# Kernel optimization log

Hardware: AMD Instinct MI355X
Metric: run time of the kernel (lower is better)

Reference implementation:

```python
import jax, jax.numpy as jnp
import numpy as np

N = 50000   # nodes
E = 800000  # edges
D = 128     # input_dim == hidden_dim
R = 8       # num_relations
B = 2       # num_blocks


def setup_inputs() -> dict:
    key = jax.random.key(0)
    ks = jax.random.split(key, 9)
    x = jax.random.normal(ks[0], (N, D), dtype=jnp.float32)
    edge_index = jax.random.randint(ks[1], (2, E), 0, N, dtype=jnp.int32)
    edge_type = jax.random.randint(ks[2], (E,), 0, R, dtype=jnp.int32)
    s_blk = 1.0 / np.sqrt(D // B)
    s_root = 1.0 / np.sqrt(D)
    W1 = jax.random.normal(ks[3], (R, B, D // B, D // B), dtype=jnp.float32) * s_blk
    root1 = jax.random.normal(ks[4], (D, D), dtype=jnp.float32) * s_root
    b1 = jnp.zeros((D,), dtype=jnp.float32)
    W2 = jax.random.normal(ks[5], (R, B, D // B, D // B), dtype=jnp.float32) * s_blk
    root2 = jax.random.normal(ks[6], (D, D), dtype=jnp.float32) * s_root
    b2 = jnp.zeros((D,), dtype=jnp.float32)
    return {"x": x, "edge_index": edge_index, "edge_type": edge_type,
            "W1": W1, "root1": root1, "b1": b1,
            "W2": W2, "root2": root2, "b2": b2}


def rgcn_conv(x, src, dst, etype, W, root, bias):
    # PyG RGCNConv (num_blocks mode): per-relation MEAN aggregation of source
    # features, block-diagonal transform, summed over relations, plus root + bias.
    # Transform is linear, so aggregate first (saves per-edge matmuls).
    n = x.shape[0]
    r, b, ib, ob = W.shape
    xs = x[src]                                   # [E, d_in] gather
    seg = dst * r + etype                          # fused (node, relation) id
    sums = jax.ops.segment_sum(xs, seg, num_segments=n * r)        # [n*r, d_in]
    cnt = jax.ops.segment_sum(jnp.ones((xs.shape[0],), xs.dtype), seg,
                              num_segments=n * r)                   # [n*r]
    mean = sums / jnp.maximum(cnt, 1.0)[:, None]   # zero where no edges
    agg = mean.reshape(n, r, b, ib)                # [n, R, blocks, in/blocks]
    out = jnp.einsum('nrbc,rbcd->nbd', agg, W).reshape(n, b * ob)
    return out + x @ root + bias


def reference(x, edge_index, edge_type, W1, root1, b1, W2, root2, b2):
    src, dst = edge_index[0], edge_index[1]
    h = jax.nn.relu(rgcn_conv(x, src, dst, edge_type, W1, root1, b1))
    # dropout(p=0.2) is identity in eval mode (reference uses eval semantics)
    return rgcn_conv(h, src, dst, edge_type, W2, root2, b2)
```

## Files before the change

### kernel.cpp

```cpp
#include <hip/hip_runtime.h>

#define NN 50000
#define EE 800000
#define DD 128
#define RR 8
#define CELLS (NN * RR)
#define TILE_N 64
#define NBLK ((NN + TILE_N - 1) / TILE_N)
#define SCAN_CHUNK 1024
#define SCAN_BLOCKS ((CELLS + SCAN_CHUNK - 1) / SCAN_CHUNK)

typedef __attribute__((ext_vector_type(4))) float f32x4;
typedef __attribute__((ext_vector_type(8))) short s16x8;
union ABu { uint4 q; s16x8 v; };


__device__ __forceinline__ unsigned int packbf2(float a, float b) {
    unsigned int ua = __float_as_uint(a);
    unsigned int ub = __float_as_uint(b);
    ua = (ua + 0x7fffu + ((ua >> 16) & 1u)) >> 16;
    ub = (ub + 0x7fffu + ((ub >> 16) & 1u)) & 0xffff0000u;
    return ua | ub;
}

__device__ __forceinline__ void upadd16(float* sA, uint4 a, uint4 b) {
    unsigned int u[8] = {a.x, a.y, a.z, a.w, b.x, b.y, b.z, b.w};
#pragma unroll
    for (int j = 0; j < 8; ++j) {
        sA[2 * j]     += __uint_as_float(u[j] << 16);
        sA[2 * j + 1] += __uint_as_float(u[j] & 0xffff0000u);
    }
}

#define NB_A ((NN * 32 + 255) / 256)
#define NB_B 128
#define NB_C 32
#define NB_D ((EE + 255) / 256)

__global__ void prep_fused(const float* __restrict__ x, unsigned int* __restrict__ xb,
                           const float* __restrict__ W1, const float* __restrict__ W2,
                           unsigned int* __restrict__ Wb1, unsigned int* __restrict__ Wb2,
                           const float* __restrict__ r1, const float* __restrict__ r2,
                           unsigned int* __restrict__ rb1, unsigned int* __restrict__ rb2,
                           const int* __restrict__ dst, const int* __restrict__ et,
                           int* __restrict__ cnt) {
    int bid = blockIdx.x, tid = threadIdx.x;
    if (bid < NB_A) {
        int i = bid * 256 + tid;
        if (i < NN * 32) {
            float4 v = ((const float4*)x)[i];
            ((uint2*)xb)[i] = make_uint2(packbf2(v.x, v.y), packbf2(v.z, v.w));
        }
    } else if (bid < NB_A + NB_B) {
        int i = (bid - NB_A) * 256 + tid;
        int n = i & 63, kp = (i >> 6) & 31, rb = i >> 11;
        int s0 = (rb * 64 + 2 * kp) * 64 + n;
        int s1 = (rb * 64 + 2 * kp + 1) * 64 + n;
        Wb1[((rb * 64 + n) * 32) + kp] = packbf2(W1[s0], W1[s1]);
        Wb2[((rb * 64 + n) * 32) + kp] = packbf2(W2[s0], W2[s1]);
    } else if (bid < NB_A + NB_B + NB_C) {
        int i = (bid - NB_A - NB_B) * 256 + tid;
        int n = i & 127, kp = i >> 7;
        int s0 = (2 * kp) * 128 + n, s1 = (2 * kp + 1) * 128 + n;
        rb1[n * 64 + kp] = packbf2(r1[s0], r1[s1]);
        rb2[n * 64 + kp] = packbf2(r2[s0], r2[s1]);
    } else {
        int e = (bid - NB_A - NB_B - NB_C) * 256 + tid;
        if (e < EE) atomicAdd(&cnt[et[e] * NN + dst[e]], 1);
    }
}


__global__ __launch_bounds__(256) void scan1(const int* __restrict__ cnt,
                                             int* __restrict__ off, int* __restrict__ bsum) {
    __shared__ int s[256];
    int tid = threadIdx.x;
    int base = blockIdx.x * SCAN_CHUNK + tid * 4;
    int v[4];
#pragma unroll
    for (int i = 0; i < 4; ++i) v[i] = (base + i < CELLS) ? cnt[base + i] : 0;
    int tot = v[0] + v[1] + v[2] + v[3];
    s[tid] = tot;
    __syncthreads();
    for (int d = 1; d < 256; d <<= 1) {
        int t = (tid >= d) ? s[tid - d] : 0;
        __syncthreads();
        s[tid] += t;
        __syncthreads();
    }
    int excl = s[tid] - tot;
    if (tid == 255) bsum[blockIdx.x] = s[255];
    int run = excl;
#pragma unroll
    for (int i = 0; i < 4; ++i) {
        if (base + i < CELLS) off[base + i] = run;
        run += v[i];
    }
}

__global__ __launch_bounds__(256) void scan3(int* __restrict__ off, const int* __restrict__ bsum,
                                             int* __restrict__ cur) {
    __shared__ int red[256];
    int tid = threadIdx.x, bid = blockIdx.x;
    int a = 0;
    for (int i = tid; i < bid; i += 256) a += bsum[i];
    red[tid] = a;
    __syncthreads();
#pragma unroll
    for (int d = 128; d > 0; d >>= 1) {
        if (tid < d) red[tid] += red[tid + d];
        __syncthreads();
    }
    int add = red[0];
    int base = bid * SCAN_CHUNK + tid * 4;
#pragma unroll
    for (int i = 0; i < 4; ++i) {
        int c = base + i;
        if (c < CELLS) {
            int o = off[c] + add;
            off[c] = o;
            cur[c] = o;
        }
    }
    if (bid == 0 && tid == 0) off[CELLS] = EE;
}

__global__ void cell_scatter(const int* __restrict__ src, const int* __restrict__ dst,
                             const int* __restrict__ et, int* __restrict__ cur,
                             int* __restrict__ esrc) {
    int e = blockIdx.x * blockDim.x + threadIdx.x;
    if (e < EE) {
        int cell = et[e] * NN + dst[e];
        int pos = atomicAdd(&cur[cell], 1);
        esrc[pos] = src[e];
    }
}

__global__ __launch_bounds__(512, 8) void gather_cells(
    const unsigned int* __restrict__ xgb, const int* __restrict__ esrc,
    const int* __restrict__ off, unsigned int* __restrict__ AT) {

    int bid = blockIdx.x;
    int r = bid / NBLK, tb = bid - r * NBLK;
    int n0 = tb * TILE_N;
    int tid = threadIdx.x;
    int e = tid & 63, q = tid >> 6;
    int node = n0 + e;

    float sA[16];
#pragma unroll
    for (int i = 0; i < 16; ++i) sA[i] = 0.f;

    int ne = 0;
    if (node < NN) {
        int cell = r * NN + node;
        int o = off[cell];
        ne = off[cell + 1] - o;
        int t2 = 0;
        for (; t2 + 2 <= ne; t2 += 2) {
            int s0 = esrc[o + t2], s1 = esrc[o + t2 + 1];
            const uint4* p0 = (const uint4*)(xgb + (size_t)s0 * 64 + q * 8);
            const uint4* p1 = (const uint4*)(xgb + (size_t)s1 * 64 + q * 8);
            uint4 A0 = p0[0], A1 = p0[1];
            uint4 B0 = p1[0], B1 = p1[1];
            upadd16(sA, A0, A1);
            upadd16(sA, B0, B1);
        }
        if (t2 < ne) {
            int s0 = esrc[o + t2];
            const uint4* p0 = (const uint4*)(xgb + (size_t)s0 * 64 + q * 8);
            uint4 A0 = p0[0], A1 = p0[1];
            upadd16(sA, A0, A1);
        }
    }
    float sc = 1.0f / (float)max(ne, 1);

    unsigned int* dst = AT + ((size_t)bid << 12);
#pragma unroll
    for (int i = 0; i < 8; ++i)
        dst[(8 * q + i) * 64 + e] = packbf2(sA[2 * i] * sc, sA[2 * i + 1] * sc);
}

template <int RELU, int WRITEF, int WRITEB>
__global__ __launch_bounds__(512, 4) void gemm_fused(
    const unsigned int* __restrict__ xgb, const unsigned int* __restrict__ AT,
    const unsigned int* __restrict__ Wb, const unsigned int* __restrict__ rootb,
    const float* __restrict__ bias, float* __restrict__ outf,
    unsigned int* __restrict__ outb) {

    __shared__ unsigned int SH[8320];
    unsigned int* MT = SH;

    int tid = threadIdx.x;
    int tb = blockIdx.x;
    int n0 = tb * TILE_N;
    int e = tid & 63, q = tid >> 6;
    int w = q, l = e;
    int quad = l >> 4, li = l & 15;
    int b = w >> 2;
    int nloc = (w & 3) * 16 + li;

    f32x4 acc[4];
    {
        float bb = bias[16 * w + li];
#pragma unroll
        for (int mt = 0; mt < 4; ++mt) {
            acc[mt][0] = bb; acc[mt][1] = bb; acc[mt][2] = bb; acc[mt][3] = bb;
        }
    }

    int node = n0 + e;

#define MFMA_BLOCK(rr) do {                                                           \
    const uint4* WbB = (const uint4*)(Wb + (((size_t)(rr) * 2 + b) * 64) * 32);       \
    _Pragma("unroll") for (int kc = 0; kc < 2; ++kc) {                                \
        ABu bf; bf.q = WbB[nloc * 8 + 4 * kc + quad];                                 \
        _Pragma("unroll") for (int mt = 0; mt < 4; ++mt) {                            \
            ABu af; int base_ = (32 * b + 16 * kc + 4 * quad) * 67 + 16 * mt + li;    \
            af.q.x = MT[base_];       af.q.y = MT[base_ + 67];                        \
            af.q.z = MT[base_ + 134]; af.q.w = MT[base_ + 201];                       \
            acc[mt] = __builtin_amdgcn_mfma_f32_16x16x32_bf16(af.v, bf.v, acc[mt], 0, 0, 0); \
        } } } while (0)

#pragma unroll
    for (int r = 0; r < RR; ++r) {
        const unsigned int* at = AT + (((size_t)(r * NBLK + tb)) << 12) + (8 * q) * 64 + e;
        unsigned int tv[8];
#pragma unroll
        for (int i = 0; i < 8; ++i) tv[i] = at[i * 64];

        __syncthreads();
#pragma unroll
        for (int i = 0; i < 8; ++i) MT[(8 * q + i) * 67 + e] = tv[i];
        __syncthreads();
        MFMA_BLOCK(r);
    }
    __syncthreads();

    if (node < NN) {
        const uint4* xr = (const uint4*)(xgb + (size_t)node * 64 + q * 8);
        uint4 X0 = xr[0], X1 = xr[1];
        MT[(8 * q + 0) * 67 + e] = X0.x;
        MT[(8 * q + 1) * 67 + e] = X0.y;
        MT[(8 * q + 2) * 67 + e] = X0.z;
        MT[(8 * q + 3) * 67 + e] = X0.w;
        MT[(8 * q + 4) * 67 + e] = X1.x;
        MT[(8 * q + 5) * 67 + e] = X1.y;
        MT[(8 * q + 6) * 67 + e] = X1.z;
        MT[(8 * q + 7) * 67 + e] = X1.w;
    } else {
#pragma unroll
        for (int i = 0; i < 8; ++i) MT[(8 * q + i) * 67 + e] = 0u;
    }
    __syncthreads();

    const uint4* RbB = (const uint4*)rootb;
#pragma unroll
    for (int kc = 0; kc < 4; ++kc) {
        ABu bf;
        bf.q = RbB[(16 * w + li) * 16 + 4 * kc + quad];
#pragma unroll
        for (int mt = 0; mt < 4; ++mt) {
            ABu af;
            int base = (16 * kc + 4 * quad) * 67 + 16 * mt + li;
            af.q.x = MT[base]; af.q.y = MT[base + 67];
            af.q.z = MT[base + 134]; af.q.w = MT[base + 201];
            acc[mt] = __builtin_amdgcn_mfma_f32_16x16x32_bf16(af.v, bf.v, acc[mt], 0, 0, 0);
        }
    }
    __syncthreads();

    float* OF = (float*)SH;
#pragma unroll
    for (int mt = 0; mt < 4; ++mt)
#pragma unroll
        for (int reg = 0; reg < 4; ++reg)
            OF[(16 * mt + 4 * quad + reg) * 130 + 16 * w + li] = acc[mt][reg];
    __syncthreads();

    if (WRITEB) {
        int p = tid & 63, rg = tid >> 6;
#pragma unroll 4
        for (int it = 0; it < 8; ++it) {
            int ee = it * 8 + rg, row = n0 + ee;
            if (row < NN) {
                float v0 = OF[ee * 130 + 2 * p], v1 = OF[ee * 130 + 2 * p + 1];
                if (RELU) { v0 = fmaxf(v0, 0.f); v1 = fmaxf(v1, 0.f); }
                outb[(size_t)row * 64 + p] = packbf2(v0, v1);
            }
        }
    }
    if (WRITEF) {
        int d4 = (tid & 31) * 4, rg = tid >> 5;
#pragma unroll 4
        for (int it = 0; it < 4; ++it) {
            int ee = it * 16 + rg, row = n0 + ee;
            if (row < NN) {
                float4 v = make_float4(OF[ee * 130 + d4], OF[ee * 130 + d4 + 1],
                                       OF[ee * 130 + d4 + 2], OF[ee * 130 + d4 + 3]);
                if (RELU) {
                    v.x = fmaxf(v.x, 0.f); v.y = fmaxf(v.y, 0.f);
                    v.z = fmaxf(v.z, 0.f); v.w = fmaxf(v.w, 0.f);
                }
                *(float4*)(outf + (size_t)row * DD + d4) = v;
            }
        }
    }
#undef MFMA_BLOCK
}


extern "C" void kernel_launch(void* const* d_in, const int* in_sizes, int n_in,
                              void* d_out, int out_size, void* d_ws, size_t ws_size,
                              hipStream_t stream) {
    const float* x     = (const float*)d_in[0];
    const int*   ei    = (const int*)d_in[1];
    const int*   src   = ei;
    const int*   dstp  = ei + EE;
    const int*   et    = (const int*)d_in[2];
    const float* W1    = (const float*)d_in[3];
    const float* root1 = (const float*)d_in[4];
    const float* b1    = (const float*)d_in[5];
    const float* W2    = (const float*)d_in[6];
    const float* root2 = (const float*)d_in[7];
    const float* b2    = (const float*)d_in[8];
    float* out = (float*)d_out;

    unsigned int* xb  = (unsigned int*)d_ws;
    unsigned int* hb  = xb + (size_t)NN * 64;
    int* cnt  = (int*)(hb + (size_t)NN * 64);
    int* off  = cnt + CELLS;
    int* cur  = off + CELLS + 1;
    int* bsum = cur + CELLS;
    int* esrc = bsum + 512;
    unsigned int* Wb1 = (unsigned int*)(esrc + EE);
    unsigned int* Wb2 = Wb1 + 32768;
    unsigned int* rb1 = Wb2 + 32768;
    unsigned int* rb2 = rb1 + 8192;
    unsigned int* AT  = rb2 + 8192;

    hipMemsetAsync(cnt, 0, CELLS * sizeof(int), stream);
    prep_fused<<<NB_A + NB_B + NB_C + NB_D, 256, 0, stream>>>(
        x, xb, W1, W2, Wb1, Wb2, root1, root2, rb1, rb2, dstp, et, cnt);
    scan1<<<SCAN_BLOCKS, 256, 0, stream>>>(cnt, off, bsum);
    scan3<<<SCAN_BLOCKS, 256, 0, stream>>>(off, bsum, cur);
    cell_scatter<<<(EE + 255) / 256, 256, 0, stream>>>(src, dstp, et, cur, esrc);

    gather_cells<<<RR * NBLK, 512, 0, stream>>>(xb, esrc, off, AT);
    gemm_fused<1, 0, 1><<<NBLK, 512, 0, stream>>>(xb, AT, Wb1, rb1, b1, nullptr, hb);
    gather_cells<<<RR * NBLK, 512, 0, stream>>>(hb, esrc, off, AT);
    gemm_fused<0, 1, 0><<<NBLK, 512, 0, stream>>>(hb, AT, Wb2, rb2, b2, out, nullptr);
}
```

Baseline: 345.2 us.

## Remap gather threads so each node row is read by eight contiguous lanes

Changes the gather kernel's thread mapping so 8 consecutive lanes load one source node's full 256-byte bf16 row, instead of each lane handling a different node. The aggregated AT tile is now stored row-major with 16-byte vector stores, and the GEMM kernel reads it (and x) with matching vector loads before transposing into shared memory. The aim is more coalesced global traffic in the random-gather kernel and the intermediate. In exchange, each wave covers fewer nodes, and the shared-memory store pattern and bank conflicts change.

Measured after the change: 329.4 us. 4.6% less time.

```diff
diff --git a/kernel.cpp b/kernel.cpp
--- a/kernel.cpp
+++ b/kernel.cpp
@@ -144,8 +144,10 @@
     int r = bid / NBLK, tb = bid - r * NBLK;
     int n0 = tb * TILE_N;
     int tid = threadIdx.x;
-    int e = tid & 63, q = tid >> 6;
-    int node = n0 + e;
+    int w = tid >> 6, l = tid & 63;
+    int g = l >> 3, qq = l & 7;
+    int nl = 8 * w + g;
+    int node = n0 + nl;
 
     float sA[16];
 #pragma unroll
@@ -159,8 +161,8 @@
         int t2 = 0;
         for (; t2 + 2 <= ne; t2 += 2) {
             int s0 = esrc[o + t2], s1 = esrc[o + t2 + 1];
-            const uint4* p0 = (const uint4*)(xgb + (size_t)s0 * 64 + q * 8);
-            const uint4* p1 = (const uint4*)(xgb + (size_t)s1 * 64 + q * 8);
+            const uint4* p0 = (const uint4*)(xgb + (size_t)s0 * 64 + qq * 8);
+            const uint4* p1 = (const uint4*)(xgb + (size_t)s1 * 64 + qq * 8);
             uint4 A0 = p0[0], A1 = p0[1];
             uint4 B0 = p1[0], B1 = p1[1];
             upadd16(sA, A0, A1);
@@ -168,17 +170,19 @@
         }
         if (t2 < ne) {
             int s0 = esrc[o + t2];
-            const uint4* p0 = (const uint4*)(xgb + (size_t)s0 * 64 + q * 8);
+            const uint4* p0 = (const uint4*)(xgb + (size_t)s0 * 64 + qq * 8);
             uint4 A0 = p0[0], A1 = p0[1];
             upadd16(sA, A0, A1);
         }
     }
     float sc = 1.0f / (float)max(ne, 1);
 
-    unsigned int* dst = AT + ((size_t)bid << 12);
-#pragma unroll
-    for (int i = 0; i < 8; ++i)
-        dst[(8 * q + i) * 64 + e] = packbf2(sA[2 * i] * sc, sA[2 * i + 1] * sc);
+    unsigned int ob[8];
+#pragma unroll
+    for (int i = 0; i < 8; ++i) ob[i] = packbf2(sA[2 * i] * sc, sA[2 * i + 1] * sc);
+    uint4* dst = (uint4*)(AT + ((size_t)bid << 12) + nl * 64 + qq * 8);
+    dst[0] = make_uint4(ob[0], ob[1], ob[2], ob[3]);
+    dst[1] = make_uint4(ob[4], ob[5], ob[6], ob[7]);
 }
 
 template <int RELU, int WRITEF, int WRITEB>
@@ -199,6 +203,7 @@
     int quad = l >> 4, li = l & 15;
     int b = w >> 2;
     int nloc = (w & 3) * 16 + li;
+    int g2 = l >> 3, q2 = l & 7, nl2 = 8 * w + g2;
 
     f32x4 acc[4];
     {
@@ -208,8 +213,6 @@
             acc[mt][0] = bb; acc[mt][1] = bb; acc[mt][2] = bb; acc[mt][3] = bb;
         }
     }
-
-    int node = n0 + e;
 
 #define MFMA_BLOCK(rr) do {                                                           \
     const uint4* WbB = (const uint4*)(Wb + (((size_t)(rr) * 2 + b) * 64) * 32);       \
@@ -224,33 +227,40 @@
 
 #pragma unroll
     for (int r = 0; r < RR; ++r) {
-        const unsigned int* at = AT + (((size_t)(r * NBLK + tb)) << 12) + (8 * q) * 64 + e;
-        unsigned int tv[8];
-#pragma unroll
-        for (int i = 0; i < 8; ++i) tv[i] = at[i * 64];
-
-        __syncthreads();
-#pragma unroll
-        for (int i = 0; i < 8; ++i) MT[(8 * q + i) * 67 + e] = tv[i];
+        const uint4* at = (const uint4*)(AT + (((size_t)(r * NBLK + tb)) << 12) + nl2 * 64 + q2 * 8);
+        uint4 X0 = at[0], X1 = at[1];
+
+        __syncthreads();
+        MT[(8 * q2 + 0) * 67 + nl2] = X0.x;
+        MT[(8 * q2 + 1) * 67 + nl2] = X0.y;
+        MT[(8 * q2 + 2) * 67 + nl2] = X0.z;
+        MT[(8 * q2 + 3) * 67 + nl2] = X0.w;
+        MT[(8 * q2 + 4) * 67 + nl2] = X1.x;
+        MT[(8 * q2 + 5) * 67 + nl2] = X1.y;
+        MT[(8 * q2 + 6) * 67 + nl2] = X1.z;
+        MT[(8 * q2 + 7) * 67 + nl2] = X1.w;
         __syncthreads();
         MFMA_BLOCK(r);
     }
     __syncthreads();
 
-    if (node < NN) {
-        const uint4* xr = (const uint4*)(xgb + (size_t)node * 64 + q * 8);
-        uint4 X0 = xr[0], X1 = xr[1];
-        MT[(8 * q + 0) * 67 + e] = X0.x;
-        MT[(8 * q + 1) * 67 + e] = X0.y;
-        MT[(8 * q + 2) * 67 + e] = X0.z;
-        MT[(8 * q + 3) * 67 + e] = X0.w;
-        MT[(8 * q + 4) * 67 + e] = X1.x;
-        MT[(8 * q + 5) * 67 + e] = X1.y;
-        MT[(8 * q + 6) * 67 + e] = X1.z;
-        MT[(8 * q + 7) * 67 + e] = X1.w;
-    } else {
-#pragma unroll
-        for (int i = 0; i < 8; ++i) MT[(8 * q + i) * 67 + e] = 0u;
+    {
+        int nodeg = n0 + nl2;
+        if (nodeg < NN) {
+            const uint4* xr = (const uint4*)(xgb + (size_t)nodeg * 64 + q2 * 8);
+            uint4 X0 = xr[0], X1 = xr[1];
+            MT[(8 * q2 + 0) * 67 + nl2] = X0.x;
+            MT[(8 * q2 + 1) * 67 + nl2] = X0.y;
+            MT[(8 * q2 + 2) * 67 + nl2] = X0.z;
+            MT[(8 * q2 + 3) * 67 + nl2] = X0.w;
+            MT[(8 * q2 + 4) * 67 + nl2] = X1.x;
+            MT[(8 * q2 + 5) * 67 + nl2] = X1.y;
+            MT[(8 * q2 + 6) * 67 + nl2] = X1.z;
+            MT[(8 * q2 + 7) * 67 + nl2] = X1.w;
+        } else {
+#pragma unroll
+            for (int i = 0; i < 8; ++i) MT[(8 * q2 + i) * 67 + nl2] = 0u;
+        }
     }
     __syncthreads();
 
```
